# Kernel tuning notes

Hardware: AMD Instinct MI355X
Metric: run time of the kernel (lower is better)

## Reference

```python
import jax, jax.numpy as jnp
import numpy as np

B, C, CI, HM, HC = 4, 64, 32, 128, 64  # batch, in_channels, inter_channels, main HW, cross HW
BN_EPS = 1e-5


def conv1x1(x, w, b):
    # x: [B,Cin,H,W], w: [Cout,Cin], b: [Cout]
    return jnp.einsum('bchw,oc->bohw', x, w) + b[None, :, None, None]


def _lin_coords(n_in, n_out):
    # PyTorch bilinear, align_corners=False: src = (i+0.5)*scale - 0.5, clamped
    scale = n_in / n_out
    src = (jnp.arange(n_out, dtype=jnp.float32) + 0.5) * scale - 0.5
    src = jnp.clip(src, 0.0, n_in - 1)
    i0 = jnp.floor(src).astype(jnp.int32)
    i1 = jnp.minimum(i0 + 1, n_in - 1)
    w = src - i0.astype(jnp.float32)
    return i0, i1, w


def resize_bilinear(x, h_out, w_out):
    # x: [B,C,H,W] -> [B,C,h_out,w_out], matches torch F.interpolate(mode='bilinear', align_corners=False)
    _, _, h_in, w_in = x.shape
    i0, i1, wh = _lin_coords(h_in, h_out)
    x = x[:, :, i0, :] * (1.0 - wh)[None, None, :, None] + x[:, :, i1, :] * wh[None, None, :, None]
    j0, j1, ww = _lin_coords(w_in, w_out)
    x = x[:, :, :, j0] * (1.0 - ww)[None, None, None, :] + x[:, :, :, j1] * ww[None, None, None, :]
    return x


def setup_inputs() -> dict:
    key = jax.random.key(0)
    ks = jax.random.split(key, 12)
    p = lambda k, shape, s=0.05: jax.random.normal(k, shape, dtype=jnp.float32) * s
    return {
        'main_feature': jax.random.normal(ks[0], (B, C, HM, HM), dtype=jnp.float32),
        'cross_feature': jax.random.normal(ks[1], (B, C, HC, HC), dtype=jnp.float32),
        'g_w': p(ks[2], (CI, C)), 'g_b': p(ks[3], (CI,)),
        'theta_w': p(ks[4], (CI, C)), 'theta_b': p(ks[5], (CI,)),
        'phi_w': p(ks[6], (CI, C)), 'phi_b': p(ks[7], (CI,)),
        'w_w': p(ks[8], (C, CI)), 'w_b': p(ks[9], (C,)),
        'bn_gamma': 1.0 + p(ks[10], (C,)), 'bn_beta': p(ks[11], (C,)),
    }


def reference(main_feature, cross_feature, g_w, g_b, theta_w, theta_b,
              phi_w, phi_b, w_w, w_b, bn_gamma, bn_beta):
    b, _, hc, wc = cross_feature.shape
    hm = main_feature.shape[2]
    # g(cross) -> [B, Nc, Ci]
    x = conv1x1(cross_feature, g_w, g_b).reshape(b, CI, -1).transpose(0, 2, 1)
    # theta(cross) -> [B, Ci, Nc]
    y = conv1x1(cross_feature, theta_w, theta_b).reshape(b, CI, -1)
    # phi(resize(main -> cross size)) -> [B, Nc, Ci]
    z = resize_bilinear(main_feature, hc, hc)
    z = conv1x1(z, phi_w, phi_b).reshape(b, CI, -1).transpose(0, 2, 1)
    # unscaled attention: [B, Nc, Nc]
    f = jnp.einsum('bnc,bcm->bnm', x, y)
    attn = jax.nn.softmax(f, axis=-1)
    out = jnp.einsum('bnm,bmc->bnc', attn, z)           # [B, Nc, Ci]
    out = out.transpose(0, 2, 1).reshape(b, CI, hc, wc)  # [B, Ci, Hc, Wc]
    # W: 1x1 conv + BatchNorm2d (training mode: batch statistics, biased var)
    out = conv1x1(out, w_w, w_b)
    mean = out.mean(axis=(0, 2, 3), keepdims=True)
    var = out.var(axis=(0, 2, 3), keepdims=True)
    out = (out - mean) * jax.lax.rsqrt(var + BN_EPS)
    out = out * bn_gamma[None, :, None, None] + bn_beta[None, :, None, None]
    out = resize_bilinear(out, hm, hm)
    return out + main_feature
```

## Files before the change

### kernel.cpp

```cpp
#include <hip/hip_runtime.h>
#include <hip/hip_bf16.h>


typedef __attribute__((ext_vector_type(8))) short bf16x8;
typedef __attribute__((ext_vector_type(4))) float f32x4;
typedef __attribute__((ext_vector_type(16))) float f32x16;

#define LOG2E 1.4426950408889634f

static __device__ __forceinline__ unsigned short f2bf_bits(float x) {
    __hip_bfloat16 h = __float2bfloat16(x);
    return *(unsigned short*)&h;
}
static __device__ __forceinline__ unsigned int pk2bf(float a, float b) {
    __hip_bfloat162 h = __float22bfloat162_rn(make_float2(a, b));
    return *(unsigned int*)&h;
}

static __device__ __forceinline__ void softmax_pack(
    const f32x16& s, float& den, bf16x8& ap1, bf16x8& ap2)
{
    float e[16];
#pragma unroll
    for (int r = 0; r < 16; ++r) e[r] = __builtin_amdgcn_exp2f(s[r]);
    den += (((e[0]+e[1])+(e[2]+e[3])) + ((e[4]+e[5])+(e[6]+e[7])))
         + (((e[8]+e[9])+(e[10]+e[11])) + ((e[12]+e[13])+(e[14]+e[15])));
    uint4 t1 = make_uint4(pk2bf(e[0],e[1]), pk2bf(e[2],e[3]),
                          pk2bf(e[4],e[5]), pk2bf(e[6],e[7]));
    uint4 t2 = make_uint4(pk2bf(e[8],e[9]), pk2bf(e[10],e[11]),
                          pk2bf(e[12],e[13]), pk2bf(e[14],e[15]));
    ap1 = *(bf16x8*)&t1; ap2 = *(bf16x8*)&t2;
}

__global__ __launch_bounds__(256) void qkv_kernel(
    const float* __restrict__ cross, const float* __restrict__ mainf,
    const float* __restrict__ g_w,  const float* __restrict__ g_b,
    const float* __restrict__ th_w, const float* __restrict__ th_b,
    const float* __restrict__ ph_w, const float* __restrict__ ph_b,
    __hip_bfloat16* __restrict__ Qb, __hip_bfloat16* __restrict__ Kb,
    __hip_bfloat16* __restrict__ Vt)
{
    __shared__ float xs[64][128];
    const int kind = blockIdx.x >> 7;
    const int sub  = blockIdx.x & 127;
    const int b    = sub >> 5;
    const int n0   = (sub & 31) << 7;
    const int tid  = threadIdx.x;
    const float* w  = (kind == 0) ? g_w : (kind == 1) ? th_w : ph_w;
    const float* bs = (kind == 0) ? g_b : (kind == 1) ? th_b : ph_b;

    if (kind < 2) {
        const float* src = cross + (((size_t)(b * 64)) << 12) + n0;
        const int jr = (tid & 31) << 2, c0 = tid >> 5;
#pragma unroll
        for (int it = 0; it < 8; ++it) {
            int c = (it << 3) | c0;
            *(float4*)&xs[c][jr] = *(const float4*)(src + ((size_t)c << 12) + jr);
        }
    } else {
        const int px = tid & 127, chh = tid >> 7;
        const int n = n0 + px;
        const int i2 = (n >> 6) << 1, j2 = (n & 63) << 1;
        const float* src = mainf + (((size_t)(b * 64)) << 14) + i2 * 128 + j2;
#pragma unroll 4
        for (int cc = 0; cc < 32; ++cc) {
            int c = (chh << 5) | cc;
            const float2 a = *(const float2*)(src + ((size_t)c << 14));
            const float2 d = *(const float2*)(src + ((size_t)c << 14) + 128);
            xs[c][px] = 0.25f * ((a.x + a.y) + (d.x + d.y));
        }
    }
    __syncthreads();

    const int px = tid & 127, cih = tid >> 7, ci0 = cih << 4;
    float acc[16];
#pragma unroll
    for (int j = 0; j < 16; ++j) acc[j] = bs[ci0 + j];
#pragma unroll 4
    for (int c = 0; c < 64; ++c) {
        float x = xs[c][px];
#pragma unroll
        for (int j = 0; j < 16; ++j)
            acc[j] = fmaf(w[((ci0 + j) << 6) + c], x, acc[j]);
    }
    const int n = n0 + px;
    const int pix = (b << 12) + n;
    if (kind < 2) {
        if (kind == 0) {
#pragma unroll
            for (int j = 0; j < 16; ++j) acc[j] *= LOG2E;
        }
        unsigned int u[8];
#pragma unroll
        for (int i = 0; i < 8; ++i)
            u[i] = (unsigned int)f2bf_bits(acc[2 * i]) |
                   ((unsigned int)f2bf_bits(acc[2 * i + 1]) << 16);
        uint4* d4 = (uint4*)(((kind == 0) ? Qb : Kb) + (size_t)pix * 32 + ci0);
        d4[0] = make_uint4(u[0], u[1], u[2], u[3]);
        d4[1] = make_uint4(u[4], u[5], u[6], u[7]);
    } else {
#pragma unroll
        for (int j = 0; j < 16; ++j)
            Vt[((size_t)((b << 5) | (ci0 + j)) << 12) + n] = __float2bfloat16(acc[j]);
    }
}

__global__ __launch_bounds__(256) void attn_part(
    const __hip_bfloat16* __restrict__ Qb, const __hip_bfloat16* __restrict__ Kb,
    const __hip_bfloat16* __restrict__ Vt,
    float* __restrict__ pnum, float* __restrict__ pden)
{
    __shared__ __align__(16) float redbuf[4][3][64][20];
    const int tid = threadIdx.x, lane = tid & 63, w = tid >> 6;
    const int q = lane & 31, h = lane >> 5;
    const int b = blockIdx.y, qbase = blockIdx.x << 7, quarter = blockIdx.z;
    const int sig = (q & ~12) | ((q & 4) << 1) | ((q & 8) >> 1);

    const __hip_bfloat16* QrowA = Qb + (((size_t)(b << 12) + qbase + q) << 5);
    const bf16x8 bq1A = *(const bf16x8*)(QrowA + 8 * h);
    const bf16x8 bq2A = *(const bf16x8*)(QrowA + 16 + 8 * h);
    const bf16x8 bq1B = *(const bf16x8*)(QrowA + (32 << 5) + 8 * h);
    const bf16x8 bq2B = *(const bf16x8*)(QrowA + (32 << 5) + 16 + 8 * h);
    const bf16x8 bq1C = *(const bf16x8*)(QrowA + (64 << 5) + 8 * h);
    const bf16x8 bq2C = *(const bf16x8*)(QrowA + (64 << 5) + 16 + 8 * h);
    const bf16x8 bq1D = *(const bf16x8*)(QrowA + (96 << 5) + 8 * h);
    const bf16x8 bq2D = *(const bf16x8*)(QrowA + (96 << 5) + 16 + 8 * h);

    const __hip_bfloat16* Kbb = Kb + ((size_t)(b << 12) << 5);
    const __hip_bfloat16* Vbb = Vt + ((size_t)(b << 5) << 12) + ((size_t)q << 12);
    const int kq = (quarter << 10) + (w << 8);
#define LDK1(k) (*(const bf16x8*)(Kbb + ((size_t)((k) + sig) << 5) + 8 * h))
#define LDK2(k) (*(const bf16x8*)(Kbb + ((size_t)((k) + sig) << 5) + 16 + 8 * h))
#define LDV1(k) (*(const bf16x8*)(Vbb + (k) + 8 * h))
#define LDV2(k) (*(const bf16x8*)(Vbb + (k) + 16 + 8 * h))

    f32x16 accA, accB, accC, accD;
#pragma unroll
    for (int r = 0; r < 16; ++r) { accA[r]=0.f; accB[r]=0.f; accC[r]=0.f; accD[r]=0.f; }
    const f32x16 z16 = accA;
    float denA = 0.f, denB = 0.f, denC = 0.f, denD = 0.f;

    bf16x8 a1c = LDK1(kq),      a2c = LDK2(kq);
    bf16x8 vb1 = LDV1(kq),      vb2 = LDV2(kq);
    bf16x8 a1n = LDK1(kq + 32), a2n = LDK2(kq + 32);
    bf16x8 vn1 = LDV1(kq + 32), vn2 = LDV2(kq + 32);
    bf16x8 apA1, apA2, apB1, apB2, apC1, apC2, apD1, apD2, vp1, vp2;

    {
        f32x16 s = __builtin_amdgcn_mfma_f32_32x32x16_bf16(a1c, bq1A, z16, 0, 0, 0);
        s = __builtin_amdgcn_mfma_f32_32x32x16_bf16(a2c, bq2A, s, 0, 0, 0);
        softmax_pack(s, denA, apA1, apA2);
        s = __builtin_amdgcn_mfma_f32_32x32x16_bf16(a1c, bq1B, z16, 0, 0, 0);
        s = __builtin_amdgcn_mfma_f32_32x32x16_bf16(a2c, bq2B, s, 0, 0, 0);
        softmax_pack(s, denB, apB1, apB2);
        s = __builtin_amdgcn_mfma_f32_32x32x16_bf16(a1c, bq1C, z16, 0, 0, 0);
        s = __builtin_amdgcn_mfma_f32_32x32x16_bf16(a2c, bq2C, s, 0, 0, 0);
        softmax_pack(s, denC, apC1, apC2);
        s = __builtin_amdgcn_mfma_f32_32x32x16_bf16(a1c, bq1D, z16, 0, 0, 0);
        s = __builtin_amdgcn_mfma_f32_32x32x16_bf16(a2c, bq2D, s, 0, 0, 0);
        softmax_pack(s, denD, apD1, apD2);
    }

#pragma unroll 2
    for (int ch = 1; ch < 8; ++ch) {
        const int kn = kq + ((ch + 1) & 7) * 32;
        vp1 = vb1; vp2 = vb2;
        vb1 = vn1; vb2 = vn2;
        a1c = a1n; a2c = a2n;
        a1n = LDK1(kn); a2n = LDK2(kn);
        vn1 = LDV1(kn); vn2 = LDV2(kn);

        accA = __builtin_amdgcn_mfma_f32_32x32x16_bf16(apA1, vp1, accA, 0, 0, 0);
        accA = __builtin_amdgcn_mfma_f32_32x32x16_bf16(apA2, vp2, accA, 0, 0, 0);
        accB = __builtin_amdgcn_mfma_f32_32x32x16_bf16(apB1, vp1, accB, 0, 0, 0);
        accB = __builtin_amdgcn_mfma_f32_32x32x16_bf16(apB2, vp2, accB, 0, 0, 0);
        accC = __builtin_amdgcn_mfma_f32_32x32x16_bf16(apC1, vp1, accC, 0, 0, 0);
        accC = __builtin_amdgcn_mfma_f32_32x32x16_bf16(apC2, vp2, accC, 0, 0, 0);
        accD = __builtin_amdgcn_mfma_f32_32x32x16_bf16(apD1, vp1, accD, 0, 0, 0);
        accD = __builtin_amdgcn_mfma_f32_32x32x16_bf16(apD2, vp2, accD, 0, 0, 0);

        f32x16 s = __builtin_amdgcn_mfma_f32_32x32x16_bf16(a1c, bq1A, z16, 0, 0, 0);
        s = __builtin_amdgcn_mfma_f32_32x32x16_bf16(a2c, bq2A, s, 0, 0, 0);
        softmax_pack(s, denA, apA1, apA2);
        s = __builtin_amdgcn_mfma_f32_32x32x16_bf16(a1c, bq1B, z16, 0, 0, 0);
        s = __builtin_amdgcn_mfma_f32_32x32x16_bf16(a2c, bq2B, s, 0, 0, 0);
        softmax_pack(s, denB, apB1, apB2);
        s = __builtin_amdgcn_mfma_f32_32x32x16_bf16(a1c, bq1C, z16, 0, 0, 0);
        s = __builtin_amdgcn_mfma_f32_32x32x16_bf16(a2c, bq2C, s, 0, 0, 0);
        softmax_pack(s, denC, apC1, apC2);
        s = __builtin_amdgcn_mfma_f32_32x32x16_bf16(a1c, bq1D, z16, 0, 0, 0);
        s = __builtin_amdgcn_mfma_f32_32x32x16_bf16(a2c, bq2D, s, 0, 0, 0);
        softmax_pack(s, denD, apD1, apD2);
    }
    accA = __builtin_amdgcn_mfma_f32_32x32x16_bf16(apA1, vb1, accA, 0, 0, 0);
    accA = __builtin_amdgcn_mfma_f32_32x32x16_bf16(apA2, vb2, accA, 0, 0, 0);
    accB = __builtin_amdgcn_mfma_f32_32x32x16_bf16(apB1, vb1, accB, 0, 0, 0);
    accB = __builtin_amdgcn_mfma_f32_32x32x16_bf16(apB2, vb2, accB, 0, 0, 0);
    accC = __builtin_amdgcn_mfma_f32_32x32x16_bf16(apC1, vb1, accC, 0, 0, 0);
    accC = __builtin_amdgcn_mfma_f32_32x32x16_bf16(apC2, vb2, accC, 0, 0, 0);
    accD = __builtin_amdgcn_mfma_f32_32x32x16_bf16(apD1, vb1, accD, 0, 0, 0);
    accD = __builtin_amdgcn_mfma_f32_32x32x16_bf16(apD2, vb2, accD, 0, 0, 0);
#undef LDK1
#undef LDK2
#undef LDV1
#undef LDV2

    denA += __shfl_xor(denA, 32);
    denB += __shfl_xor(denB, 32);
    denC += __shfl_xor(denC, 32);
    denD += __shfl_xor(denD, 32);

    if (w) {
        float d[4] = {denA, denB, denC, denD};
        const f32x16* av[4] = {&accA, &accB, &accC, &accD};
#pragma unroll
        for (int T = 0; T < 4; ++T) {
            float* rb = &redbuf[T][w - 1][lane][0];
            f32x4* rb4 = (f32x4*)rb;
            const f32x16& a = *av[T];
#pragma unroll
            for (int p = 0; p < 4; ++p) {
                f32x4 t = {a[4*p], a[4*p+1], a[4*p+2], a[4*p+3]};
                rb4[p] = t;
            }
            rb[16] = d[T];
        }
    }
    __syncthreads();
    if (w == 0) {
        const int tbase = (((quarter << 2) | b) << 7) | (blockIdx.x << 2);
        float d[4] = {denA, denB, denC, denD};
        f32x16* av[4] = {&accA, &accB, &accC, &accD};
#pragma unroll
        for (int T = 0; T < 4; ++T) {
            f32x16& a = *av[T];
#pragma unroll
            for (int ww = 0; ww < 3; ++ww) {
                const float* rb = &redbuf[T][ww][lane][0];
                const f32x4* rb4 = (const f32x4*)rb;
#pragma unroll
                for (int p = 0; p < 4; ++p) {
                    f32x4 t = rb4[p];
                    a[4*p] += t[0]; a[4*p+1] += t[1];
                    a[4*p+2] += t[2]; a[4*p+3] += t[3];
                }
                d[T] += rb[16];
            }
            float* pn = pnum + ((size_t)(tbase + T) << 10);
#pragma unroll
            for (int r = 0; r < 16; ++r) {
                int qr = (r & 3) + 8 * (r >> 2) + 4 * h;
                pn[(qr << 5) + q] = a[r];
            }
            if (h == 0) pden[((tbase + T) << 5) + q] = d[T];
        }
    }
}

__global__ __launch_bounds__(256) void attn_combine(
    const float* __restrict__ pnum, const float* __restrict__ pden,
    const float* __restrict__ w_w, const float* __restrict__ w_b,
    float* __restrict__ out2, float2* __restrict__ pstats)
{
    __shared__ __align__(16) float obuf[32][36];
    const int tid = threadIdx.x;
    const int b = blockIdx.y, qbase = blockIdx.x << 5;

#pragma unroll
    for (int k = 0; k < 4; ++k) {
        int e = tid + (k << 8);
        int qr = e >> 5;
        float num = 0.f, den = 0.f;
#pragma unroll
        for (int quarter = 0; quarter < 4; ++quarter) {
            int tile = (((quarter << 2) | b) << 7) | blockIdx.x;
            num += pnum[((size_t)tile << 10) + e];
            den += pden[(tile << 5) + qr];
        }
        obuf[qr][e & 31] = num * (1.0f / den);
    }
    __syncthreads();

    const int qq = tid & 31, cog = tid >> 5;
    float ov[32];
    const float4* orow = (const float4*)&obuf[qq][0];
#pragma unroll
    for (int k4 = 0; k4 < 8; ++k4) {
        float4 t = orow[k4];
        ov[4*k4] = t.x; ov[4*k4+1] = t.y; ov[4*k4+2] = t.z; ov[4*k4+3] = t.w;
    }
    float* dstbase = out2 + (((size_t)(b << 6)) << 12) + qbase + qq;
    const int tileidx = (b << 7) | blockIdx.x;
#pragma unroll
    for (int kk = 0; kk < 8; ++kk) {
        int co = (kk << 3) | cog;
        const float4* wr = (const float4*)&w_w[co << 5];
        float acc2 = w_b[co];
#pragma unroll
        for (int k4 = 0; k4 < 8; ++k4) {
            float4 t = wr[k4];
            acc2 = fmaf(t.x, ov[4*k4],   acc2);
            acc2 = fmaf(t.y, ov[4*k4+1], acc2);
            acc2 = fmaf(t.z, ov[4*k4+2], acc2);
            acc2 = fmaf(t.w, ov[4*k4+3], acc2);
        }
        dstbase[(size_t)co << 12] = acc2;
        float s1 = acc2, s2 = acc2 * acc2;
#pragma unroll
        for (int m = 1; m < 32; m <<= 1) {
            s1 += __shfl_xor(s1, m);
            s2 += __shfl_xor(s2, m);
        }
        if (qq == 0) pstats[(co << 9) | tileidx] = make_float2(s1, s2);
    }
}

__global__ __launch_bounds__(256) void up_kernel(
    const float* __restrict__ out2, const float2* __restrict__ pstats,
    const float* __restrict__ gamma, const float* __restrict__ beta,
    const float* __restrict__ mainf, float* __restrict__ out)
{
    int gid = blockIdx.x * 256 + threadIdx.x;
    int j4 = (gid & 31) << 2;
    int i  = (gid >> 5) & 127;
    int co = (gid >> 12) & 63;
    int b  = gid >> 18;
    int t  = threadIdx.x;

    __shared__ float rs[256], rs2[256];
    {
        float2 p0 = pstats[(co << 9) | t];
        float2 p1 = pstats[(co << 9) | (t + 256)];
        rs[t] = p0.x + p1.x; rs2[t] = p0.y + p1.y;
    }
    __syncthreads();
    for (int off = 128; off > 0; off >>= 1) {
        if (t < off) { rs[t] += rs[t + off]; rs2[t] += rs2[t + off]; }
        __syncthreads();
    }
    float sm = rs[0], sq = rs2[0];

    float mean = sm * (1.0f / 16384.0f);
    float var  = sq * (1.0f / 16384.0f) - mean * mean;
    float inv  = rsqrtf(var + 1e-5f);
    float scale = gamma[co] * inv;
    float shift = beta[co] - mean * scale;

    int ih = i >> 1;
    int k0, k1; float wi;
    if (i & 1)       { k0 = ih;     k1 = (ih < 63) ? ih + 1 : 63; wi = 0.25f; }
    else if (ih == 0){ k0 = 0;      k1 = 0;                       wi = 0.0f;  }
    else             { k0 = ih - 1; k1 = ih;                      wi = 0.75f; }

    const float* p0r = out2 + ((size_t)((b << 6) | co) << 12) + (k0 << 6);
    const float* p1r = out2 + ((size_t)((b << 6) | co) << 12) + (k1 << 6);

    float res[4];
#pragma unroll
    for (int jj = 0; jj < 4; ++jj) {
        int j = j4 | jj;
        int il = j >> 1;
        int l0, l1; float wj;
        if (j & 1)       { l0 = il;     l1 = (il < 63) ? il + 1 : 63; wj = 0.25f; }
        else if (il == 0){ l0 = 0;      l1 = 0;                       wj = 0.0f;  }
        else             { l0 = il - 1; l1 = il;                      wj = 0.75f; }
        float v00 = p0r[l0], v01 = p0r[l1];
        float v10 = p1r[l0], v11 = p1r[l1];
        float top = v00 + wj * (v01 - v00);
        float bot = v10 + wj * (v11 - v10);
        float v = top + wi * (bot - top);
        res[jj] = fmaf(v, scale, shift);
    }
    size_t idx = (((size_t)((b << 6) | co)) << 14) + (i << 7) + j4;
    float4 m4 = *(const float4*)(mainf + idx);
    *(float4*)(out + idx) = make_float4(res[0] + m4.x, res[1] + m4.y,
                                        res[2] + m4.z, res[3] + m4.w);
}

extern "C" void kernel_launch(void* const* d_in, const int* in_sizes, int n_in,
                              void* d_out, int out_size, void* d_ws, size_t ws_size,
                              hipStream_t stream)
{
    const float* mainf = (const float*)d_in[0];
    const float* cross = (const float*)d_in[1];
    const float* g_w   = (const float*)d_in[2];
    const float* g_b   = (const float*)d_in[3];
    const float* th_w  = (const float*)d_in[4];
    const float* th_b  = (const float*)d_in[5];
    const float* ph_w  = (const float*)d_in[6];
    const float* ph_b  = (const float*)d_in[7];
    const float* w_w   = (const float*)d_in[8];
    const float* w_b   = (const float*)d_in[9];
    const float* gamma = (const float*)d_in[10];
    const float* beta  = (const float*)d_in[11];
    float* out = (float*)d_out;

    __hip_bfloat16* Qb = (__hip_bfloat16*)d_ws;
    __hip_bfloat16* Kb = Qb + 524288;
    __hip_bfloat16* Vt = Kb + 524288;
    float* out2   = (float*)(Vt + 524288);
    float* pnum   = out2 + 1048576;
    float* pden   = pnum + 2097152;
    float2* pstats = (float2*)(pden + 65536);

    qkv_kernel<<<384, 256, 0, stream>>>(cross, mainf, g_w, g_b, th_w, th_b,
                                        ph_w, ph_b, Qb, Kb, Vt);
    attn_part<<<dim3(32, 4, 4), 256, 0, stream>>>(Qb, Kb, Vt, pnum, pden);
    attn_combine<<<dim3(128, 4), 256, 0, stream>>>(pnum, pden, w_w, w_b,
                                                   out2, pstats);
    up_kernel<<<4096, 256, 0, stream>>>(out2, pstats, gamma, beta, mainf, out);
}
```

Baseline: 144.7 us.

## Pre-swizzle K and V into per-chunk MFMA fragment layout for coalesced loads

```diff
diff --git a/kernel.cpp b/kernel.cpp
--- a/kernel.cpp
+++ b/kernel.cpp
@@ -37,8 +37,8 @@
     const float* __restrict__ g_w,  const float* __restrict__ g_b,
     const float* __restrict__ th_w, const float* __restrict__ th_b,
     const float* __restrict__ ph_w, const float* __restrict__ ph_b,
-    __hip_bfloat16* __restrict__ Qb, __hip_bfloat16* __restrict__ Kb,
-    __hip_bfloat16* __restrict__ Vt)
+    __hip_bfloat16* __restrict__ Qb, __hip_bfloat16* __restrict__ Kf,
+    __hip_bfloat16* __restrict__ Vf)
 {
     __shared__ float xs[64][128];
     const int kind = blockIdx.x >> 7;
@@ -84,37 +84,48 @@
             acc[j] = fmaf(w[((ci0 + j) << 6) + c], x, acc[j]);
     }
     const int n = n0 + px;
-    const int pix = (b << 12) + n;
-    if (kind < 2) {
-        if (kind == 0) {
-#pragma unroll
-            for (int j = 0; j < 16; ++j) acc[j] *= LOG2E;
-        }
+    const int chunk = n >> 5, kk = n & 31;
+    if (kind == 0) {
+#pragma unroll
+        for (int j = 0; j < 16; ++j) acc[j] *= LOG2E;
         unsigned int u[8];
 #pragma unroll
         for (int i = 0; i < 8; ++i)
             u[i] = (unsigned int)f2bf_bits(acc[2 * i]) |
                    ((unsigned int)f2bf_bits(acc[2 * i + 1]) << 16);
-        uint4* d4 = (uint4*)(((kind == 0) ? Qb : Kb) + (size_t)pix * 32 + ci0);
+        uint4* d4 = (uint4*)(Qb + (size_t)((b << 12) + n) * 32 + ci0);
         d4[0] = make_uint4(u[0], u[1], u[2], u[3]);
         d4[1] = make_uint4(u[4], u[5], u[6], u[7]);
+    } else if (kind == 1) {
+        unsigned int u[8];
+#pragma unroll
+        for (int i = 0; i < 8; ++i)
+            u[i] = (unsigned int)f2bf_bits(acc[2 * i]) |
+                   ((unsigned int)f2bf_bits(acc[2 * i + 1]) << 16);
+        const int q = (kk & ~12) | ((kk & 4) << 1) | ((kk & 8) >> 1);
+        char* base = (char*)Kf + ((((size_t)(b << 7) | chunk) << 11) | (cih << 10));
+        *(uint4*)(base + (q << 4))          = make_uint4(u[0], u[1], u[2], u[3]);
+        *(uint4*)(base + ((32 + q) << 4))   = make_uint4(u[4], u[5], u[6], u[7]);
     } else {
-#pragma unroll
-        for (int j = 0; j < 16; ++j)
-            Vt[((size_t)((b << 5) | (ci0 + j)) << 12) + n] = __float2bfloat16(acc[j]);
+        const int j = (kk >> 4) & 1, hh = (kk >> 3) & 1, e = kk & 7;
+        char* base = (char*)Vf + ((((size_t)(b << 7) | chunk) << 11) | (j << 10) | (e << 1));
+#pragma unroll
+        for (int jj = 0; jj < 16; ++jj) {
+            int ci = ci0 + jj;
+            *(unsigned short*)(base + (((hh << 5) | ci) << 4)) = f2bf_bits(acc[jj]);
+        }
     }
 }
 
 __global__ __launch_bounds__(256) void attn_part(
-    const __hip_bfloat16* __restrict__ Qb, const __hip_bfloat16* __restrict__ Kb,
-    const __hip_bfloat16* __restrict__ Vt,
+    const __hip_bfloat16* __restrict__ Qb, const __hip_bfloat16* __restrict__ Kf,
+    const __hip_bfloat16* __restrict__ Vf,
     float* __restrict__ pnum, float* __restrict__ pden)
 {
     __shared__ __align__(16) float redbuf[4][3][64][20];
     const int tid = threadIdx.x, lane = tid & 63, w = tid >> 6;
     const int q = lane & 31, h = lane >> 5;
     const int b = blockIdx.y, qbase = blockIdx.x << 7, quarter = blockIdx.z;
-    const int sig = (q & ~12) | ((q & 4) << 1) | ((q & 8) >> 1);
 
     const __hip_bfloat16* QrowA = Qb + (((size_t)(b << 12) + qbase + q) << 5);
     const bf16x8 bq1A = *(const bf16x8*)(QrowA + 8 * h);
@@ -126,13 +137,14 @@
     const bf16x8 bq1D = *(const bf16x8*)(QrowA + (96 << 5) + 8 * h);
     const bf16x8 bq2D = *(const bf16x8*)(QrowA + (96 << 5) + 16 + 8 * h);
 
-    const __hip_bfloat16* Kbb = Kb + ((size_t)(b << 12) << 5);
-    const __hip_bfloat16* Vbb = Vt + ((size_t)(b << 5) << 12) + ((size_t)q << 12);
-    const int kq = (quarter << 10) + (w << 8);
-#define LDK1(k) (*(const bf16x8*)(Kbb + ((size_t)((k) + sig) << 5) + 8 * h))
-#define LDK2(k) (*(const bf16x8*)(Kbb + ((size_t)((k) + sig) << 5) + 16 + 8 * h))
-#define LDV1(k) (*(const bf16x8*)(Vbb + (k) + 8 * h))
-#define LDV2(k) (*(const bf16x8*)(Vbb + (k) + 16 + 8 * h))
+    const char* Kc = (const char*)Kf +
+        ((size_t)((b << 7) | (quarter << 5) | (w << 3)) << 11) + (lane << 4);
+    const char* Vc = (const char*)Vf +
+        ((size_t)((b << 7) | (quarter << 5) | (w << 3)) << 11) + (lane << 4);
+#define LDK1(c) (*(const bf16x8*)(Kc + ((c) << 11)))
+#define LDK2(c) (*(const bf16x8*)(Kc + ((c) << 11) + 1024))
+#define LDV1(c) (*(const bf16x8*)(Vc + ((c) << 11)))
+#define LDV2(c) (*(const bf16x8*)(Vc + ((c) << 11) + 1024))
 
     f32x16 accA, accB, accC, accD;
 #pragma unroll
@@ -140,10 +152,10 @@
     const f32x16 z16 = accA;
     float denA = 0.f, denB = 0.f, denC = 0.f, denD = 0.f;
 
-    bf16x8 a1c = LDK1(kq),      a2c = LDK2(kq);
-    bf16x8 vb1 = LDV1(kq),      vb2 = LDV2(kq);
-    bf16x8 a1n = LDK1(kq + 32), a2n = LDK2(kq + 32);
-    bf16x8 vn1 = LDV1(kq + 32), vn2 = LDV2(kq + 32);
+    bf16x8 a1c = LDK1(0), a2c = LDK2(0);
+    bf16x8 vb1 = LDV1(0), vb2 = LDV2(0);
+    bf16x8 a1n = LDK1(1), a2n = LDK2(1);
+    bf16x8 vn1 = LDV1(1), vn2 = LDV2(1);
     bf16x8 apA1, apA2, apB1, apB2, apC1, apC2, apD1, apD2, vp1, vp2;
 
     {
@@ -163,7 +175,7 @@
 
 #pragma unroll 2
     for (int ch = 1; ch < 8; ++ch) {
-        const int kn = kq + ((ch + 1) & 7) * 32;
+        const int kn = (ch + 1) & 7;
         vp1 = vb1; vp2 = vb2;
         vb1 = vn1; vb2 = vn2;
         a1c = a1n; a2c = a2n;
@@ -396,16 +408,16 @@
     float* out = (float*)d_out;
 
     __hip_bfloat16* Qb = (__hip_bfloat16*)d_ws;
-    __hip_bfloat16* Kb = Qb + 524288;
-    __hip_bfloat16* Vt = Kb + 524288;
-    float* out2   = (float*)(Vt + 524288);
+    __hip_bfloat16* Kf = Qb + 524288;
+    __hip_bfloat16* Vf = Kf + 524288;
+    float* out2   = (float*)(Vf + 524288);
     float* pnum   = out2 + 1048576;
     float* pden   = pnum + 2097152;
     float2* pstats = (float2*)(pden + 65536);
 
     qkv_kernel<<<384, 256, 0, stream>>>(cross, mainf, g_w, g_b, th_w, th_b,
-                                        ph_w, ph_b, Qb, Kb, Vt);
-    attn_part<<<dim3(32, 4, 4), 256, 0, stream>>>(Qb, Kb, Vt, pnum, pden);
+                                        ph_w, ph_b, Qb, Kf, Vf);
+    attn_part<<<dim3(32, 4, 4), 256, 0, stream>>>(Qb, Kf, Vf, pnum, pden);
     attn_combine<<<dim3(128, 4), 256, 0, stream>>>(pnum, pden, w_w, w_b,
                                                    out2, pstats);
     up_kernel<<<4096, 256, 0, stream>>>(out2, pstats, gamma, beta, mainf, out);
```

Result: no change. 143.5 us (-0.9%).
